# Kernel optimization log

Hardware: AMD Instinct MI355X
Metric: run time of the kernel (lower is better)

The kernel has to match this reference:

```python
import jax, jax.numpy as jnp
import numpy as np
from jax import lax

B, H, N, D = 8, 8, 4096, 64
NUM_LANDMARKS = 256
PINV_ITERS = 6
KERNEL = 33


def moore_penrose_iter_pinv(x, iters=PINV_ITERS):
    # x: [b, h, m, m]
    abs_x = jnp.abs(x)
    col = abs_x.sum(axis=-1)
    row = abs_x.sum(axis=-2)
    z = jnp.swapaxes(x, -1, -2) / (jnp.max(col) * jnp.max(row))
    I = jnp.eye(x.shape[-1], dtype=x.dtype)
    for _ in range(iters):
        xz = x @ z
        z = 0.25 * z @ (13.0 * I - xz @ (15.0 * I - xz @ (7.0 * I - xz)))
    return z


def setup_inputs() -> dict:
    key = jax.random.key(0)
    ks = jax.random.split(key, 10)
    inp = {
        'q': jax.random.normal(ks[0], (B, H, N, D), dtype=jnp.float32),
        'k': jax.random.normal(ks[1], (B, H, N, D), dtype=jnp.float32),
        'v': jax.random.normal(ks[2], (B, H, N, D), dtype=jnp.float32),
        'Wsim1': jax.random.uniform(ks[3], (H, H), dtype=jnp.float32),
        'Wsim2': jax.random.uniform(ks[4], (H, H), dtype=jnp.float32),
        'Wsim3': jax.random.uniform(ks[5], (H, H), dtype=jnp.float32),
        'Wattn1': jax.random.uniform(ks[6], (H, H), dtype=jnp.float32),
        'Wattn2': jax.random.uniform(ks[7], (H, H), dtype=jnp.float32),
        'Wattn3': jax.random.uniform(ks[8], (H, H), dtype=jnp.float32),
        'conv_w': jax.random.normal(ks[9], (H, H, KERNEL, 1), dtype=jnp.float32) * 0.05,
    }
    return inp


def reference(q, k, v, Wsim1, Wsim2, Wsim3, Wattn1, Wattn2, Wattn3, conv_w):
    b, h, n, d = q.shape
    # m = max(12, min(num_landmarks, int((sqrt(kn) + sqrt(qn)) // 2))) -> 64 for n=4096
    m = max(12, min(NUM_LANDMARKS, int((n ** 0.5 + n ** 0.5) // 2)))
    l = -(-n // m)  # ceil(n / m); n % m == 0 here so no padding branch

    # landmarks: group-sum over l consecutive tokens, divided by l
    q_l = q.reshape(b, h, m, l, d).sum(axis=3) / l  # [b,h,m,d]
    k_l = k.reshape(b, h, m, l, d).sum(axis=3) / l  # [b,h,m,d]

    sim1 = jnp.einsum('bhid,bhjd->bhij', q, k_l)    # [b,h,n,m]
    sim2 = jnp.einsum('bhid,bhjd->bhij', q_l, k_l)  # [b,h,m,m]
    sim3 = jnp.einsum('bhid,bhjd->bhij', q_l, k)    # [b,h,m,n]

    # talking-head mixing on sims
    sim1 = jnp.einsum('bhij,hk->bkij', sim1, Wsim1)
    sim2 = jnp.einsum('bhij,hk->bkij', sim2, Wsim2)
    sim3 = jnp.einsum('bhij,hk->bkij', sim3, Wsim3)

    attn1 = jax.nn.softmax(sim1, axis=-1)
    attn2 = jax.nn.softmax(sim2, axis=-1)
    attn3 = jax.nn.softmax(sim3, axis=-1)

    attn2_inv = moore_penrose_iter_pinv(attn2, PINV_ITERS)

    # talking-head mixing on attns
    attn1 = jnp.einsum('bhij,hk->bkij', attn1, Wattn1)
    attn2_inv = jnp.einsum('bhij,hk->bkij', attn2_inv, Wattn2)
    attn3 = jnp.einsum('bhij,hk->bkij', attn3, Wattn3)

    out = attn1 @ (attn2_inv @ (attn3 @ v))  # [b,h,n,d]

    # residual depthwise-ish conv over (n, d) treating heads as channels
    pad = KERNEL // 2
    res = lax.conv_general_dilated(
        v, conv_w,
        window_strides=(1, 1),
        padding=[(pad, pad), (0, 0)],
        dimension_numbers=('NCHW', 'OIHW', 'NCHW'))
    out = out + res
    return out
```

## Files before the change

### kernel.cpp

```cpp
#include <hip/hip_runtime.h>
#include <cstddef>
#include <cstdint>

constexpr int cB = 8, cH = 8, cN = 4096, cD = 64, cM = 64, cL = 64;

__global__ void k_landmarks(const float* __restrict__ q, const float* __restrict__ k,
                            float* __restrict__ ql, float* __restrict__ kl) {
  int bm = blockIdx.x;
  int bh = bm >> 6, m = bm & 63;
  int d = threadIdx.x;
  size_t base = ((size_t)bh * cN + (size_t)m * cL) * cD + d;
  float sq = 0.f, sk = 0.f;
  for (int t = 0; t < cL; ++t) {
    sq += q[base + (size_t)t * cD];
    sk += k[base + (size_t)t * cD];
  }
  size_t ob = ((size_t)bh * cM + m) * cD + d;
  ql[ob] = sq * (1.0f / cL);
  kl[ob] = sk * (1.0f / cL);
}

__global__ void __launch_bounds__(256) k_sim2(const float* __restrict__ ql,
                                              const float* __restrict__ kl,
                                              const float* __restrict__ Wsim2,
                                              float* __restrict__ attn2,
                                              unsigned int* __restrict__ scal) {
  __shared__ float qs[64][65];
  __shared__ float ks[64][65];
  __shared__ float acc[64 * 65];
  int b = blockIdx.x >> 3, kk = blockIdx.x & 7;
  int tid = threadIdx.x;
  for (int idx = tid; idx < 64 * 64; idx += 256)
    acc[(idx >> 6) * 65 + (idx & 63)] = 0.f;
  int ri = (tid >> 4) * 4, ci = (tid & 15) * 4;
  for (int h = 0; h < 8; ++h) {
    __syncthreads();
    const float* qg = ql + (size_t)(b * 8 + h) * 4096;
    const float* kg = kl + (size_t)(b * 8 + h) * 4096;
    for (int idx = tid; idx < 4096; idx += 256) {
      qs[idx >> 6][idx & 63] = qg[idx];
      ks[idx >> 6][idx & 63] = kg[idx];
    }
    __syncthreads();
    float w = Wsim2[h * 8 + kk];
    float s[4][4] = {};
    for (int d = 0; d < 64; ++d) {
      float a0 = qs[ri][d], a1 = qs[ri + 1][d], a2 = qs[ri + 2][d], a3 = qs[ri + 3][d];
      float b0 = ks[ci][d], b1 = ks[ci + 1][d], b2 = ks[ci + 2][d], b3 = ks[ci + 3][d];
      s[0][0] += a0 * b0; s[0][1] += a0 * b1; s[0][2] += a0 * b2; s[0][3] += a0 * b3;
      s[1][0] += a1 * b0; s[1][1] += a1 * b1; s[1][2] += a1 * b2; s[1][3] += a1 * b3;
      s[2][0] += a2 * b0; s[2][1] += a2 * b1; s[2][2] += a2 * b2; s[2][3] += a2 * b3;
      s[3][0] += a3 * b0; s[3][1] += a3 * b1; s[3][2] += a3 * b2; s[3][3] += a3 * b3;
    }
    #pragma unroll
    for (int x = 0; x < 4; ++x)
      #pragma unroll
      for (int y = 0; y < 4; ++y)
        acc[(ri + x) * 65 + ci + y] += w * s[x][y];
  }
  __syncthreads();
  if (tid < 64) {
    float mx = -1e30f;
    for (int j = 0; j < 64; ++j) mx = fmaxf(mx, acc[tid * 65 + j]);
    float s = 0.f;
    for (int j = 0; j < 64; ++j) {
      float e = expf(acc[tid * 65 + j] - mx);
      acc[tid * 65 + j] = e;
      s += e;
    }
    float inv = 1.0f / s;
    float rs = 0.f;
    for (int j = 0; j < 64; ++j) {
      float p = acc[tid * 65 + j] * inv;
      acc[tid * 65 + j] = p;
      rs += p;
    }
    atomicMax(scal + 1, __float_as_uint(rs));
  }
  __syncthreads();
  if (tid < 64) {
    float cs = 0.f;
    for (int i = 0; i < 64; ++i) cs += acc[i * 65 + tid];
    atomicMax(scal + 0, __float_as_uint(cs));
  }
  __syncthreads();
  float* op = attn2 + (size_t)(b * 8 + kk) * 4096;
  for (int idx = tid; idx < 4096; idx += 256)
    op[idx] = acc[(idx >> 6) * 65 + (idx & 63)];
}

__device__ __forceinline__ void mm64(float* __restrict__ Dst, const float* S,
                                     float c0, float c1, const float* __restrict__ P,
                                     const float* __restrict__ Q, int tid) {
  int ri = (tid >> 4) * 4, ci = (tid & 15) * 4;
  float s[4][4] = {};
  for (int k = 0; k < 64; ++k) {
    float a0 = P[(ri + 0) * 65 + k], a1 = P[(ri + 1) * 65 + k];
    float a2 = P[(ri + 2) * 65 + k], a3 = P[(ri + 3) * 65 + k];
    float b0 = Q[k * 65 + ci + 0], b1 = Q[k * 65 + ci + 1];
    float b2 = Q[k * 65 + ci + 2], b3 = Q[k * 65 + ci + 3];
    s[0][0] += a0 * b0; s[0][1] += a0 * b1; s[0][2] += a0 * b2; s[0][3] += a0 * b3;
    s[1][0] += a1 * b0; s[1][1] += a1 * b1; s[1][2] += a1 * b2; s[1][3] += a1 * b3;
    s[2][0] += a2 * b0; s[2][1] += a2 * b1; s[2][2] += a2 * b2; s[2][3] += a2 * b3;
    s[3][0] += a3 * b0; s[3][1] += a3 * b1; s[3][2] += a3 * b2; s[3][3] += a3 * b3;
  }
  #pragma unroll
  for (int x = 0; x < 4; ++x)
    #pragma unroll
    for (int y = 0; y < 4; ++y) {
      float r = c1 * s[x][y];
      if (S) r += c0 * S[(ri + x) * 65 + ci + y];
      Dst[(ri + x) * 65 + ci + y] = r;
    }
}

__global__ void __launch_bounds__(256) k_pinv(const float* __restrict__ attn2,
                                              float* __restrict__ attn2inv,
                                              const unsigned int* __restrict__ scal) {
  __shared__ float bufs[5][64 * 65];
  float* X = bufs[0];
  float* Z = bufs[1];
  float* T1 = bufs[2];
  float* T2 = bufs[3];
  float* T3 = bufs[4];
  int tid = threadIdx.x;
  const float* xg = attn2 + (size_t)blockIdx.x * 4096;
  for (int idx = tid; idx < 4096; idx += 256)
    X[(idx >> 6) * 65 + (idx & 63)] = xg[idx];
  float denom = __uint_as_float(scal[0]) * __uint_as_float(scal[1]);
  float invd = 1.0f / denom;
  __syncthreads();
  for (int idx = tid; idx < 4096; idx += 256) {
    int i = idx >> 6, j = idx & 63;
    Z[i * 65 + j] = X[j * 65 + i] * invd;
  }
  __syncthreads();
  for (int it = 0; it < 6; ++it) {
    mm64(T1, nullptr, 0.f, 1.f, X, Z, tid);          __syncthreads();
    mm64(T2, T1, 7.f, -1.f, T1, T1, tid);            __syncthreads();
    mm64(T3, T1, 15.f, -1.f, T1, T2, tid);           __syncthreads();
    mm64(T2, Z, 13.f * 0.25f, -0.25f, Z, T3, tid);   __syncthreads();
    float* tmp = Z; Z = T2; T2 = tmp;
  }
  float* og = attn2inv + (size_t)blockIdx.x * 4096;
  for (int idx = tid; idx < 4096; idx += 256)
    og[idx] = Z[(idx >> 6) * 65 + (idx & 63)];
}

__global__ void k_mix_heads64(const float* __restrict__ in, const float* __restrict__ W,
                              float* __restrict__ out) {
  int b = blockIdx.x >> 3, k2 = blockIdx.x & 7;
  int tid = threadIdx.x;
  __shared__ float w[8];
  if (tid < 8) w[tid] = W[tid * 8 + k2];
  __syncthreads();
  const float* ib = in + (size_t)b * 8 * 4096;
  float* ob = out + ((size_t)b * 8 + k2) * 4096;
  for (int idx = tid; idx < 4096; idx += 256) {
    float s = 0.f;
    #pragma unroll
    for (int k = 0; k < 8; ++k) s += ib[(size_t)k * 4096 + idx] * w[k];
    ob[idx] = s;
  }
}

__global__ void __launch_bounds__(512) k_sim3(const float* __restrict__ ql,
                                              const float* __restrict__ kg,
                                              const float* __restrict__ Wsim3,
                                              float* __restrict__ sim3m) {
  __shared__ float qls[64 * 65];
  __shared__ float ksT[64 * 36];
  __shared__ float w3[64];
  int b = blockIdx.x >> 7, jt = blockIdx.x & 127;
  int j0 = jt * 32, tid = threadIdx.x;
  if (tid < 64) w3[tid] = Wsim3[tid];
  int i = tid >> 3, jb = (tid & 7) * 4;
  float acc[8][4] = {};
  for (int h = 0; h < 8; ++h) {
    __syncthreads();
    const float* qg = ql + (size_t)(b * 8 + h) * 4096;
    for (int idx = tid; idx < 4096; idx += 512)
      qls[(idx >> 6) * 65 + (idx & 63)] = qg[idx];
    const float* kp = kg + ((size_t)(b * 8 + h) * cN + j0) * 64;
    for (int idx = tid; idx < 2048; idx += 512) {
      int j = idx >> 6, d = idx & 63;
      ksT[d * 36 + j] = kp[idx];
    }
    __syncthreads();
    float s[4] = {};
    for (int d = 0; d < 64; ++d) {
      float a = qls[i * 65 + d];
      float4 kv = *(const float4*)&ksT[d * 36 + jb];
      s[0] += a * kv.x; s[1] += a * kv.y; s[2] += a * kv.z; s[3] += a * kv.w;
    }
    #pragma unroll
    for (int k = 0; k < 8; ++k) {
      float w = w3[h * 8 + k];
      #pragma unroll
      for (int c = 0; c < 4; ++c) acc[k][c] += w * s[c];
    }
  }
  #pragma unroll
  for (int k = 0; k < 8; ++k) {
    float* op = sim3m + ((size_t)((b * 8 + k) * 64 + i)) * cN + j0 + jb;
    *(float4*)op = make_float4(acc[k][0], acc[k][1], acc[k][2], acc[k][3]);
  }
}

__global__ void k_stats3(const float* __restrict__ sim3m, float* __restrict__ rmax,
                         float* __restrict__ rsum) {
  int row = blockIdx.x;
  const float* rp = sim3m + (size_t)row * cN;
  int tid = threadIdx.x;
  float vv[16];
  float mx = -1e30f;
  #pragma unroll
  for (int t = 0; t < 16; ++t) {
    vv[t] = rp[tid + t * 256];
    mx = fmaxf(mx, vv[t]);
  }
  __shared__ float red[8];
  for (int off = 32; off > 0; off >>= 1) mx = fmaxf(mx, __shfl_down(mx, off));
  if ((tid & 63) == 0) red[tid >> 6] = mx;
  __syncthreads();
  mx = fmaxf(fmaxf(red[0], red[1]), fmaxf(red[2], red[3]));
  float s = 0.f;
  #pragma unroll
  for (int t = 0; t < 16; ++t) s += expf(vv[t] - mx);
  for (int off = 32; off > 0; off >>= 1) s += __shfl_down(s, off);
  __syncthreads();
  if ((tid & 63) == 0) red[4 + (tid >> 6)] = s;
  __syncthreads();
  if (tid == 0) {
    rmax[row] = mx;
    rsum[row] = red[4] + red[5] + red[6] + red[7];
  }
}

__global__ void __launch_bounds__(256) k_smx3(float* __restrict__ sim3m,
                                              const float* __restrict__ rmax,
                                              const float* __restrict__ rsum,
                                              const float* __restrict__ Wattn3) {
  __shared__ float w[64];
  int tid = threadIdx.x;
  if (tid < 64) w[tid] = Wattn3[tid];
  __syncthreads();
  int gid = blockIdx.x * 256 + tid;
  int j = gid & 4095;
  int i = (gid >> 12) & 63;
  int b = gid >> 18;
  float p[8];
  #pragma unroll
  for (int k = 0; k < 8; ++k) {
    int row = (b * 8 + k) * 64 + i;
    p[k] = expf(sim3m[(size_t)row * cN + j] - rmax[row]) / rsum[row];
  }
  #pragma unroll
  for (int k2 = 0; k2 < 8; ++k2) {
    float t = 0.f;
    #pragma unroll
    for (int k = 0; k < 8; ++k) t += p[k] * w[k * 8 + k2];
    int row = (b * 8 + k2) * 64 + i;
    sim3m[(size_t)row * cN + j] = t;
  }
}

__global__ void __launch_bounds__(256) k_t3(const float* __restrict__ attn3f,
                                            const float* __restrict__ v,
                                            float* __restrict__ T3p) {
  __shared__ float As[64][65];
  __shared__ float Vs[64][68];
  int bh = blockIdx.x >> 2, chunk = blockIdx.x & 3;
  int tid = threadIdx.x;
  int ri = (tid >> 4) * 4, ci = (tid & 15) * 4;
  float acc[4][4] = {};
  for (int jt = chunk * 16; jt < chunk * 16 + 16; ++jt) {
    __syncthreads();
    const float* ap = attn3f + (size_t)bh * 64 * cN + jt * 64;
    for (int idx = tid; idx < 4096; idx += 256)
      As[idx >> 6][idx & 63] = ap[(size_t)(idx >> 6) * cN + (idx & 63)];
    const float* vp = v + ((size_t)bh * cN + jt * 64) * 64;
    for (int idx = tid; idx < 4096; idx += 256)
      Vs[idx >> 6][idx & 63] = vp[idx];
    __syncthreads();
    for (int j = 0; j < 64; ++j) {
      float a0 = As[ri][j], a1 = As[ri + 1][j], a2 = As[ri + 2][j], a3 = As[ri + 3][j];
      float b0 = Vs[j][ci], b1 = Vs[j][ci + 1], b2 = Vs[j][ci + 2], b3 = Vs[j][ci + 3];
      acc[0][0] += a0 * b0; acc[0][1] += a0 * b1; acc[0][2] += a0 * b2; acc[0][3] += a0 * b3;
      acc[1][0] += a1 * b0; acc[1][1] += a1 * b1; acc[1][2] += a1 * b2; acc[1][3] += a1 * b3;
      acc[2][0] += a2 * b0; acc[2][1] += a2 * b1; acc[2][2] += a2 * b2; acc[2][3] += a2 * b3;
      acc[3][0] += a3 * b0; acc[3][1] += a3 * b1; acc[3][2] += a3 * b2; acc[3][3] += a3 * b3;
    }
  }
  float* op = T3p + ((size_t)chunk * 64 + bh) * 4096;
  #pragma unroll
  for (int x = 0; x < 4; ++x)
    #pragma unroll
    for (int y = 0; y < 4; ++y)
      op[(ri + x) * 64 + ci + y] = acc[x][y];
}

__global__ void __launch_bounds__(256) k_t2(const float* __restrict__ attn2m,
                                            const float* __restrict__ T3p,
                                            float* __restrict__ T2) {
  __shared__ float As[64][65];
  __shared__ float Bs[64][68];
  int bh = blockIdx.x, tid = threadIdx.x;
  const float* ap = attn2m + (size_t)bh * 4096;
  for (int idx = tid; idx < 4096; idx += 256) {
    As[idx >> 6][idx & 63] = ap[idx];
    float s = 0.f;
    #pragma unroll
    for (int c = 0; c < 4; ++c) s += T3p[((size_t)c * 64 + bh) * 4096 + idx];
    Bs[idx >> 6][idx & 63] = s;
  }
  __syncthreads();
  int ri = (tid >> 4) * 4, ci = (tid & 15) * 4;
  float acc[4][4] = {};
  for (int j = 0; j < 64; ++j) {
    float a0 = As[ri][j], a1 = As[ri + 1][j], a2 = As[ri + 2][j], a3 = As[ri + 3][j];
    float b0 = Bs[j][ci], b1 = Bs[j][ci + 1], b2 = Bs[j][ci + 2], b3 = Bs[j][ci + 3];
    acc[0][0] += a0 * b0; acc[0][1] += a0 * b1; acc[0][2] += a0 * b2; acc[0][3] += a0 * b3;
    acc[1][0] += a1 * b0; acc[1][1] += a1 * b1; acc[1][2] += a1 * b2; acc[1][3] += a1 * b3;
    acc[2][0] += a2 * b0; acc[2][1] += a2 * b1; acc[2][2] += a2 * b2; acc[2][3] += a2 * b3;
    acc[3][0] += a3 * b0; acc[3][1] += a3 * b1; acc[3][2] += a3 * b2; acc[3][3] += a3 * b3;
  }
  #pragma unroll
  for (int x = 0; x < 4; ++x)
    #pragma unroll
    for (int y = 0; y < 4; ++y)
      T2[(size_t)bh * 4096 + (ri + x) * 64 + ci + y] = acc[x][y];
}

__global__ void __launch_bounds__(256) k_conv(const float* __restrict__ v,
                                              const float* __restrict__ cw,
                                              float* __restrict__ out) {
  __shared__ float wl[2112];
  int tid = threadIdx.x;
  for (int idx = tid; idx < 2112; idx += 256) {
    int o = idx / 264, r = idx % 264, i = r / 33, t = r % 33;
    wl[i * 264 + t * 8 + o] = cw[idx];
  }
  __syncthreads();
  int d = tid & 63;
  int sub = tid >> 6;
  int b = blockIdx.x >> 8;
  int n0 = (blockIdx.x & 255) * 16 + sub * 4;
  float acc[8][4] = {};
  for (int i = 0; i < 8; ++i) {
    const float* vp = v + ((size_t)(b * 8 + i) * cN) * 64 + d;
    float win[36];
    #pragma unroll
    for (int t = 0; t < 36; ++t) {
      int nn = n0 - 16 + t;
      win[t] = (nn >= 0 && nn < cN) ? vp[(size_t)nn * 64] : 0.f;
    }
    #pragma unroll
    for (int t = 0; t < 33; ++t) {
      float4 w0 = *(const float4*)&wl[i * 264 + t * 8];
      float4 w1 = *(const float4*)&wl[i * 264 + t * 8 + 4];
      #pragma unroll
      for (int u = 0; u < 4; ++u) {
        float val = win[t + u];
        acc[0][u] += val * w0.x; acc[1][u] += val * w0.y;
        acc[2][u] += val * w0.z; acc[3][u] += val * w0.w;
        acc[4][u] += val * w1.x; acc[5][u] += val * w1.y;
        acc[6][u] += val * w1.z; acc[7][u] += val * w1.w;
      }
    }
  }
  #pragma unroll
  for (int o = 0; o < 8; ++o) {
    float* op = out + ((size_t)(b * 8 + o) * cN + n0) * 64 + d;
    #pragma unroll
    for (int u = 0; u < 4; ++u) op[(size_t)u * 64] = acc[o][u];
  }
}

__global__ void __launch_bounds__(512) k_final(const float* __restrict__ q,
                                               const float* __restrict__ kl,
                                               const float* __restrict__ T2,
                                               const float* __restrict__ Wsim1,
                                               const float* __restrict__ Wattn1,
                                               float* __restrict__ out) {
  __shared__ float bufS[32 * 68];
  __shared__ float bufL[64 * 68];
  __shared__ float ws1[64], wa1[64];
  int b = blockIdx.x >> 7, it = blockIdx.x & 127, i0 = it * 32, tid = threadIdx.x;
  if (tid < 64) { ws1[tid] = Wsim1[tid]; wa1[tid] = Wattn1[tid]; }
  int i = tid >> 4, jb = (tid & 15) * 4;
  float sim[8][4] = {};
  for (int h = 0; h < 8; ++h) {
    __syncthreads();
    const float* qg = q + ((size_t)(b * 8 + h) * cN + i0) * 64;
    for (int idx = tid; idx < 2048; idx += 512)
      bufS[(idx >> 6) * 68 + (idx & 63)] = qg[idx];
    const float* kg = kl + (size_t)(b * 8 + h) * 4096;
    for (int idx = tid; idx < 4096; idx += 512)
      bufL[(idx & 63) * 68 + (idx >> 6)] = kg[idx];
    __syncthreads();
    float s[4] = {};
    for (int d = 0; d < 64; ++d) {
      float a = bufS[i * 68 + d];
      float4 kv = *(const float4*)&bufL[d * 68 + jb];
      s[0] += a * kv.x; s[1] += a * kv.y; s[2] += a * kv.z; s[3] += a * kv.w;
    }
    #pragma unroll
    for (int k = 0; k < 8; ++k) {
      float wv = ws1[h * 8 + k];
      #pragma unroll
      for (int c = 0; c < 4; ++c) sim[k][c] += wv * s[c];
    }
  }
  #pragma unroll
  for (int k = 0; k < 8; ++k) {
    float mx = sim[k][0];
    #pragma unroll
    for (int c = 1; c < 4; ++c) mx = fmaxf(mx, sim[k][c]);
    mx = fmaxf(mx, __shfl_xor(mx, 1));
    mx = fmaxf(mx, __shfl_xor(mx, 2));
    mx = fmaxf(mx, __shfl_xor(mx, 4));
    mx = fmaxf(mx, __shfl_xor(mx, 8));
    float sm = 0.f;
    #pragma unroll
    for (int c = 0; c < 4; ++c) { sim[k][c] = expf(sim[k][c] - mx); sm += sim[k][c]; }
    sm += __shfl_xor(sm, 1);
    sm += __shfl_xor(sm, 2);
    sm += __shfl_xor(sm, 4);
    sm += __shfl_xor(sm, 8);
    float inv = 1.0f / sm;
    #pragma unroll
    for (int c = 0; c < 4; ++c) sim[k][c] *= inv;
  }
  #pragma unroll
  for (int c = 0; c < 4; ++c) {
    float t[8];
    #pragma unroll
    for (int k2 = 0; k2 < 8; ++k2) {
      float acc = 0.f;
      #pragma unroll
      for (int k = 0; k < 8; ++k) acc += sim[k][c] * wa1[k * 8 + k2];
      t[k2] = acc;
    }
    #pragma unroll
    for (int k2 = 0; k2 < 8; ++k2) sim[k2][c] = t[k2];
  }
  for (int k2 = 0; k2 < 8; ++k2) {
    __syncthreads();
    *(float4*)&bufS[i * 68 + jb] =
        make_float4(sim[k2][0], sim[k2][1], sim[k2][2], sim[k2][3]);
    const float* tg = T2 + (size_t)(b * 8 + k2) * 4096;
    for (int idx = tid; idx < 4096; idx += 512)
      bufL[(idx >> 6) * 68 + (idx & 63)] = tg[idx];
    __syncthreads();
    int db = jb;
    float o[4] = {};
    for (int j = 0; j < 64; ++j) {
      float p = bufS[i * 68 + j];
      float4 t = *(const float4*)&bufL[j * 68 + db];
      o[0] += p * t.x; o[1] += p * t.y; o[2] += p * t.z; o[3] += p * t.w;
    }
    float* op = out + ((size_t)(b * 8 + k2) * cN + i0 + i) * 64 + db;
    float4 e = *(float4*)op;
    e.x += o[0]; e.y += o[1]; e.z += o[2]; e.w += o[3];
    *(float4*)op = e;
  }
}

extern "C" void kernel_launch(void* const* d_in, const int* in_sizes, int n_in,
                              void* d_out, int out_size, void* d_ws, size_t ws_size,
                              hipStream_t stream) {
  const float* q = (const float*)d_in[0];
  const float* k = (const float*)d_in[1];
  const float* v = (const float*)d_in[2];
  const float* Wsim1 = (const float*)d_in[3];
  const float* Wsim2 = (const float*)d_in[4];
  const float* Wsim3 = (const float*)d_in[5];
  const float* Wattn1 = (const float*)d_in[6];
  const float* Wattn2 = (const float*)d_in[7];
  const float* Wattn3 = (const float*)d_in[8];
  const float* cw = (const float*)d_in[9];
  float* out = (float*)d_out;
  float* ws = (float*)d_ws;

  float* ql       = ws + 0;
  float* kl       = ws + 262144;
  float* attn2    = ws + 524288;
  float* attn2inv = ws + 786432;
  float* attn2m   = ws + 1048576;
  float* T2       = ws + 1310720;
  float* rmax     = ws + 1572864;
  float* rsum     = ws + 1576960;
  unsigned int* scal = (unsigned int*)(ws + 1581056);
  float* T3p      = ws + 1581120;
  float* sim3m = out;

  hipMemsetAsync(scal, 0, 8, stream);
  k_landmarks<<<dim3(4096), dim3(64), 0, stream>>>(q, k, ql, kl);
  k_sim2<<<dim3(64), dim3(256), 0, stream>>>(ql, kl, Wsim2, attn2, scal);
  k_pinv<<<dim3(64), dim3(256), 0, stream>>>(attn2, attn2inv, scal);
  k_mix_heads64<<<dim3(64), dim3(256), 0, stream>>>(attn2inv, Wattn2, attn2m);
  k_sim3<<<dim3(1024), dim3(512), 0, stream>>>(ql, k, Wsim3, sim3m);
  k_stats3<<<dim3(4096), dim3(256), 0, stream>>>(sim3m, rmax, rsum);
  k_smx3<<<dim3(8192), dim3(256), 0, stream>>>(sim3m, rmax, rsum, Wattn3);
  k_t3<<<dim3(256), dim3(256), 0, stream>>>(sim3m, v, T3p);
  k_t2<<<dim3(64), dim3(256), 0, stream>>>(attn2m, T3p, T2);
  k_conv<<<dim3(2048), dim3(256), 0, stream>>>(v, cw, out);
  k_final<<<dim3(1024), dim3(512), 0, stream>>>(q, kl, T2, Wsim1, Wattn1, out);
}
```

Before: 897.9 us.

## Double-buffer k_final with register prefetch, 2-row tiles, pre-transposed landmarks

Rewrites the final attention kernel so each block handles 64 rows, with each thread computing two rows via float4-vectorised dot products. Global loads for the next head's q/k_l (and later T2) are prefetched into registers while the current head is computed, using double-buffered shared memory so there is one barrier per step. A new small kernel transposes k_l in place so it can be loaded with coalesced float4 stores instead of a scattered transpose inside the hot kernel. The aim is to cut barriers, shared-memory traffic and load latency, at the cost of more registers and shared memory per block (occupancy hint 4) and half as many blocks.

```diff
diff --git a/kernel.cpp b/kernel.cpp
--- a/kernel.cpp
+++ b/kernel.cpp
@@ -87,6 +87,17 @@
   float* op = attn2 + (size_t)(b * 8 + kk) * 4096;
   for (int idx = tid; idx < 4096; idx += 256)
     op[idx] = acc[(idx >> 6) * 65 + (idx & 63)];
+}
+
+__global__ void k_klT(float* __restrict__ kl) {
+  __shared__ float t[64 * 65];
+  int bh = blockIdx.x, tid = threadIdx.x;
+  float* p = kl + (size_t)bh * 4096;
+  for (int idx = tid; idx < 4096; idx += 256)
+    t[(idx >> 6) * 65 + (idx & 63)] = p[idx];
+  __syncthreads();
+  for (int idx = tid; idx < 4096; idx += 256)
+    p[idx] = t[(idx & 63) * 65 + (idx >> 6)];
 }
 
 __device__ __forceinline__ void mm64(float* __restrict__ Dst, const float* S,
@@ -377,93 +388,181 @@
   }
 }
 
-__global__ void __launch_bounds__(512) k_final(const float* __restrict__ q,
-                                               const float* __restrict__ kl,
-                                               const float* __restrict__ T2,
-                                               const float* __restrict__ Wsim1,
-                                               const float* __restrict__ Wattn1,
-                                               float* __restrict__ out) {
-  __shared__ float bufS[32 * 68];
-  __shared__ float bufL[64 * 68];
+__device__ __forceinline__ void dot64_2x4(const float* __restrict__ A0,
+                                          const float* __restrict__ A1,
+                                          const float* __restrict__ Bm, int jb,
+                                          float s0[4], float s1[4]) {
+  #pragma unroll
+  for (int dc = 0; dc < 16; ++dc) {
+    float4 af0 = *(const float4*)&A0[dc * 4];
+    float4 af1 = *(const float4*)&A1[dc * 4];
+    float4 kv0 = *(const float4*)&Bm[(dc * 4 + 0) * 68 + jb];
+    float4 kv1 = *(const float4*)&Bm[(dc * 4 + 1) * 68 + jb];
+    float4 kv2 = *(const float4*)&Bm[(dc * 4 + 2) * 68 + jb];
+    float4 kv3 = *(const float4*)&Bm[(dc * 4 + 3) * 68 + jb];
+    s0[0] += af0.x * kv0.x; s0[1] += af0.x * kv0.y; s0[2] += af0.x * kv0.z; s0[3] += af0.x * kv0.w;
+    s1[0] += af1.x * kv0.x; s1[1] += af1.x * kv0.y; s1[2] += af1.x * kv0.z; s1[3] += af1.x * kv0.w;
+    s0[0] += af0.y * kv1.x; s0[1] += af0.y * kv1.y; s0[2] += af0.y * kv1.z; s0[3] += af0.y * kv1.w;
+    s1[0] += af1.y * kv1.x; s1[1] += af1.y * kv1.y; s1[2] += af1.y * kv1.z; s1[3] += af1.y * kv1.w;
+    s0[0] += af0.z * kv2.x; s0[1] += af0.z * kv2.y; s0[2] += af0.z * kv2.z; s0[3] += af0.z * kv2.w;
+    s1[0] += af1.z * kv2.x; s1[1] += af1.z * kv2.y; s1[2] += af1.z * kv2.z; s1[3] += af1.z * kv2.w;
+    s0[0] += af0.w * kv3.x; s0[1] += af0.w * kv3.y; s0[2] += af0.w * kv3.z; s0[3] += af0.w * kv3.w;
+    s1[0] += af1.w * kv3.x; s1[1] += af1.w * kv3.y; s1[2] += af1.w * kv3.z; s1[3] += af1.w * kv3.w;
+  }
+}
+
+__global__ void __launch_bounds__(512, 4) k_final(const float* __restrict__ q,
+                                                  const float* __restrict__ klT,
+                                                  const float* __restrict__ T2,
+                                                  const float* __restrict__ Wsim1,
+                                                  const float* __restrict__ Wattn1,
+                                                  float* __restrict__ out) {
+  __shared__ float SB[4 * 64 * 68];
   __shared__ float ws1[64], wa1[64];
-  int b = blockIdx.x >> 7, it = blockIdx.x & 127, i0 = it * 32, tid = threadIdx.x;
+  constexpr int PITCH = 68, BUF = 64 * 68;
+  int b = blockIdx.x >> 6, it = blockIdx.x & 63, i0 = it * 64;
+  int tid = threadIdx.x;
   if (tid < 64) { ws1[tid] = Wsim1[tid]; wa1[tid] = Wattn1[tid]; }
-  int i = tid >> 4, jb = (tid & 15) * 4;
-  float sim[8][4] = {};
+  int ip = tid >> 4, l16 = tid & 15, jb = l16 * 4, r0 = ip * 2;
+  int sr0 = tid >> 4, sc0 = (tid & 15) * 4;
+
+  float sim0[8][4] = {}, sim1[8][4] = {};
+  float4 rq0, rq1, rk0, rk1;
+
+  {
+    const float4* gq = (const float4*)(q + ((size_t)(b * 8) * cN + i0) * 64);
+    const float4* gk = (const float4*)(klT + (size_t)(b * 8) * 4096);
+    rq0 = gq[tid]; rq1 = gq[tid + 512];
+    rk0 = gk[tid]; rk1 = gk[tid + 512];
+  }
+  {
+    float* dq = SB + 0 * BUF;
+    float* dl = SB + 2 * BUF;
+    *(float4*)&dq[sr0 * PITCH + sc0] = rq0;
+    *(float4*)&dq[(32 + sr0) * PITCH + sc0] = rq1;
+    *(float4*)&dl[sr0 * PITCH + sc0] = rk0;
+    *(float4*)&dl[(32 + sr0) * PITCH + sc0] = rk1;
+  }
+  __syncthreads();
+
   for (int h = 0; h < 8; ++h) {
-    __syncthreads();
-    const float* qg = q + ((size_t)(b * 8 + h) * cN + i0) * 64;
-    for (int idx = tid; idx < 2048; idx += 512)
-      bufS[(idx >> 6) * 68 + (idx & 63)] = qg[idx];
-    const float* kg = kl + (size_t)(b * 8 + h) * 4096;
-    for (int idx = tid; idx < 4096; idx += 512)
-      bufL[(idx & 63) * 68 + (idx >> 6)] = kg[idx];
-    __syncthreads();
-    float s[4] = {};
-    for (int d = 0; d < 64; ++d) {
-      float a = bufS[i * 68 + d];
-      float4 kv = *(const float4*)&bufL[d * 68 + jb];
-      s[0] += a * kv.x; s[1] += a * kv.y; s[2] += a * kv.z; s[3] += a * kv.w;
-    }
-    #pragma unroll
-    for (int k = 0; k < 8; ++k) {
-      float wv = ws1[h * 8 + k];
+    int p = h & 1, pn = p ^ 1;
+    if (h < 7) {
+      const float4* gq = (const float4*)(q + ((size_t)(b * 8 + h + 1) * cN + i0) * 64);
+      const float4* gk = (const float4*)(klT + (size_t)(b * 8 + h + 1) * 4096);
+      rq0 = gq[tid]; rq1 = gq[tid + 512];
+      rk0 = gk[tid]; rk1 = gk[tid + 512];
+    } else {
+      const float4* gt = (const float4*)(T2 + (size_t)(b * 8) * 4096);
+      rq0 = gt[tid]; rq1 = gt[tid + 512];
+    }
+    const float* Qb = SB + p * BUF;
+    const float* Lb = SB + (2 + p) * BUF;
+    float s0[4] = {}, s1[4] = {};
+    dot64_2x4(&Qb[r0 * PITCH], &Qb[(r0 + 1) * PITCH], Lb, jb, s0, s1);
+    #pragma unroll
+    for (int kq = 0; kq < 8; ++kq) {
+      float wv = ws1[h * 8 + kq];
       #pragma unroll
-      for (int c = 0; c < 4; ++c) sim[k][c] += wv * s[c];
-    }
-  }
-  #pragma unroll
-  for (int k = 0; k < 8; ++k) {
-    float mx = sim[k][0];
-    #pragma unroll
-    for (int c = 1; c < 4; ++c) mx = fmaxf(mx, sim[k][c]);
-    mx = fmaxf(mx, __shfl_xor(mx, 1));
-    mx = fmaxf(mx, __shfl_xor(mx, 2));
-    mx = fmaxf(mx, __shfl_xor(mx, 4));
-    mx = fmaxf(mx, __shfl_xor(mx, 8));
-    float sm = 0.f;
-    #pragma unroll
-    for (int c = 0; c < 4; ++c) { sim[k][c] = expf(sim[k][c] - mx); sm += sim[k][c]; }
-    sm += __shfl_xor(sm, 1);
-    sm += __shfl_xor(sm, 2);
-    sm += __shfl_xor(sm, 4);
-    sm += __shfl_xor(sm, 8);
-    float inv = 1.0f / sm;
-    #pragma unroll
-    for (int c = 0; c < 4; ++c) sim[k][c] *= inv;
-  }
-  #pragma unroll
-  for (int c = 0; c < 4; ++c) {
-    float t[8];
-    #pragma unroll
-    for (int k2 = 0; k2 < 8; ++k2) {
-      float acc = 0.f;
+      for (int c = 0; c < 4; ++c) { sim0[kq][c] += wv * s0[c]; sim1[kq][c] += wv * s1[c]; }
+    }
+    if (h < 7) {
+      float* dq = SB + pn * BUF;
+      float* dl = SB + (2 + pn) * BUF;
+      *(float4*)&dq[sr0 * PITCH + sc0] = rq0;
+      *(float4*)&dq[(32 + sr0) * PITCH + sc0] = rq1;
+      *(float4*)&dl[sr0 * PITCH + sc0] = rk0;
+      *(float4*)&dl[(32 + sr0) * PITCH + sc0] = rk1;
+    } else {
       #pragma unroll
-      for (int k = 0; k < 8; ++k) acc += sim[k][c] * wa1[k * 8 + k2];
-      t[k2] = acc;
-    }
-    #pragma unroll
-    for (int k2 = 0; k2 < 8; ++k2) sim[k2][c] = t[k2];
-  }
+      for (int kq = 0; kq < 8; ++kq) {
+        float mx = fmaxf(fmaxf(sim0[kq][0], sim0[kq][1]), fmaxf(sim0[kq][2], sim0[kq][3]));
+        mx = fmaxf(mx, __shfl_xor(mx, 1)); mx = fmaxf(mx, __shfl_xor(mx, 2));
+        mx = fmaxf(mx, __shfl_xor(mx, 4)); mx = fmaxf(mx, __shfl_xor(mx, 8));
+        float sm = 0.f;
+        #pragma unroll
+        for (int c = 0; c < 4; ++c) { sim0[kq][c] = expf(sim0[kq][c] - mx); sm += sim0[kq][c]; }
+        sm += __shfl_xor(sm, 1); sm += __shfl_xor(sm, 2);
+        sm += __shfl_xor(sm, 4); sm += __shfl_xor(sm, 8);
+        float inv = 1.0f / sm;
+        #pragma unroll
+        for (int c = 0; c < 4; ++c) sim0[kq][c] *= inv;
+
+        float mx1 = fmaxf(fmaxf(sim1[kq][0], sim1[kq][1]), fmaxf(sim1[kq][2], sim1[kq][3]));
+        mx1 = fmaxf(mx1, __shfl_xor(mx1, 1)); mx1 = fmaxf(mx1, __shfl_xor(mx1, 2));
+        mx1 = fmaxf(mx1, __shfl_xor(mx1, 4)); mx1 = fmaxf(mx1, __shfl_xor(mx1, 8));
+        float sm1 = 0.f;
+        #pragma unroll
+        for (int c = 0; c < 4; ++c) { sim1[kq][c] = expf(sim1[kq][c] - mx1); sm1 += sim1[kq][c]; }
+        sm1 += __shfl_xor(sm1, 1); sm1 += __shfl_xor(sm1, 2);
+        sm1 += __shfl_xor(sm1, 4); sm1 += __shfl_xor(sm1, 8);
+        float inv1 = 1.0f / sm1;
+        #pragma unroll
+        for (int c = 0; c < 4; ++c) sim1[kq][c] *= inv1;
+      }
+      #pragma unroll
+      for (int c = 0; c < 4; ++c) {
+        float t0[8], t1[8];
+        #pragma unroll
+        for (int k2 = 0; k2 < 8; ++k2) {
+          float a0 = 0.f, a1 = 0.f;
+          #pragma unroll
+          for (int kk = 0; kk < 8; ++kk) {
+            float wv = wa1[kk * 8 + k2];
+            a0 += sim0[kk][c] * wv; a1 += sim1[kk][c] * wv;
+          }
+          t0[k2] = a0; t1[k2] = a1;
+        }
+        #pragma unroll
+        for (int k2 = 0; k2 < 8; ++k2) { sim0[k2][c] = t0[k2]; sim1[k2][c] = t1[k2]; }
+      }
+      float* dl = SB + 2 * BUF;
+      *(float4*)&dl[sr0 * PITCH + sc0] = rq0;
+      *(float4*)&dl[(32 + sr0) * PITCH + sc0] = rq1;
+      *(float4*)&SB[r0 * PITCH + jb] =
+          make_float4(sim0[0][0], sim0[0][1], sim0[0][2], sim0[0][3]);
+      *(float4*)&SB[(r0 + 1) * PITCH + jb] =
+          make_float4(sim1[0][0], sim1[0][1], sim1[0][2], sim1[0][3]);
+    }
+    __syncthreads();
+  }
+
+  #pragma unroll
   for (int k2 = 0; k2 < 8; ++k2) {
-    __syncthreads();
-    *(float4*)&bufS[i * 68 + jb] =
-        make_float4(sim[k2][0], sim[k2][1], sim[k2][2], sim[k2][3]);
-    const float* tg = T2 + (size_t)(b * 8 + k2) * 4096;
-    for (int idx = tid; idx < 4096; idx += 512)
-      bufL[(idx >> 6) * 68 + (idx & 63)] = tg[idx];
-    __syncthreads();
-    int db = jb;
-    float o[4] = {};
-    for (int j = 0; j < 64; ++j) {
-      float p = bufS[i * 68 + j];
-      float4 t = *(const float4*)&bufL[j * 68 + db];
-      o[0] += p * t.x; o[1] += p * t.y; o[2] += p * t.z; o[3] += p * t.w;
-    }
-    float* op = out + ((size_t)(b * 8 + k2) * cN + i0 + i) * 64 + db;
-    float4 e = *(float4*)op;
-    e.x += o[0]; e.y += o[1]; e.z += o[2]; e.w += o[3];
-    *(float4*)op = e;
+    int p = k2 & 1, pn = p ^ 1;
+    if (k2 < 7) {
+      const float4* gt = (const float4*)(T2 + (size_t)(b * 8 + k2 + 1) * 4096);
+      rq0 = gt[tid]; rq1 = gt[tid + 512];
+    }
+    const float* Pb = SB + p * BUF;
+    const float* Tb = SB + (2 + p) * BUF;
+    float o0[4] = {}, o1[4] = {};
+    dot64_2x4(&Pb[r0 * PITCH], &Pb[(r0 + 1) * PITCH], Tb, jb, o0, o1);
+    if (k2 < 7) {
+      float* dl = SB + (2 + pn) * BUF;
+      *(float4*)&dl[sr0 * PITCH + sc0] = rq0;
+      *(float4*)&dl[(32 + sr0) * PITCH + sc0] = rq1;
+      float* dp = SB + pn * BUF;
+      *(float4*)&dp[r0 * PITCH + jb] =
+          make_float4(sim0[k2 + 1][0], sim0[k2 + 1][1], sim0[k2 + 1][2], sim0[k2 + 1][3]);
+      *(float4*)&dp[(r0 + 1) * PITCH + jb] =
+          make_float4(sim1[k2 + 1][0], sim1[k2 + 1][1], sim1[k2 + 1][2], sim1[k2 + 1][3]);
+    }
+    #pragma unroll
+    for (int c = 0; c < 4; ++c) { sim0[k2][c] = o0[c]; sim1[k2][c] = o1[c]; }
+    __syncthreads();
+  }
+
+  #pragma unroll
+  for (int k2 = 0; k2 < 8; ++k2) {
+    float* op0 = out + ((size_t)(b * 8 + k2) * cN + i0 + r0) * 64 + jb;
+    float4 e0 = *(float4*)op0;
+    e0.x += sim0[k2][0]; e0.y += sim0[k2][1]; e0.z += sim0[k2][2]; e0.w += sim0[k2][3];
+    *(float4*)op0 = e0;
+    float* op1 = op0 + 64;
+    float4 e1 = *(float4*)op1;
+    e1.x += sim1[k2][0]; e1.y += sim1[k2][1]; e1.z += sim1[k2][2]; e1.w += sim1[k2][3];
+    *(float4*)op1 = e1;
   }
 }
 
@@ -498,6 +597,7 @@
   hipMemsetAsync(scal, 0, 8, stream);
   k_landmarks<<<dim3(4096), dim3(64), 0, stream>>>(q, k, ql, kl);
   k_sim2<<<dim3(64), dim3(256), 0, stream>>>(ql, kl, Wsim2, attn2, scal);
+  k_klT<<<dim3(64), dim3(256), 0, stream>>>(kl);
   k_pinv<<<dim3(64), dim3(256), 0, stream>>>(attn2, attn2inv, scal);
   k_mix_heads64<<<dim3(64), dim3(256), 0, stream>>>(attn2inv, Wattn2, attn2m);
   k_sim3<<<dim3(1024), dim3(512), 0, stream>>>(ql, k, Wsim3, sim3m);
@@ -506,5 +606,5 @@
   k_t3<<<dim3(256), dim3(256), 0, stream>>>(sim3m, v, T3p);
   k_t2<<<dim3(64), dim3(256), 0, stream>>>(attn2m, T3p, T2);
   k_conv<<<dim3(2048), dim3(256), 0, stream>>>(v, cw, out);
-  k_final<<<dim3(1024), dim3(512), 0, stream>>>(q, kl, T2, Wsim1, Wattn1, out);
-}
+  k_final<<<dim3(512), dim3(512), 0, stream>>>(q, kl, T2, Wsim1, Wattn1, out);
+}
```

New measurement: 3.500 ms. 290% more time.
